# Performance work log

Hardware: AMD Instinct MI355X
Metric: run time of the kernel (lower is better)

The kernel has to match this reference:

```python
import jax, jax.numpy as jnp
import numpy as np

N, E, QL, HID = 1024, 8192, 8, 1024
NH, NKV, HD = 16, 8, 64          # heads, kv heads, head_dim; groups = NH // NKV = 2
INTER = 4096
THETA = 10000.0
EPS = 1e-6


def rmsnorm(x, w):
    v = x.astype(jnp.float32)
    v = v * jax.lax.rsqrt(jnp.mean(v * v, axis=-1, keepdims=True) + EPS)
    return w * v.astype(x.dtype)


def rotate_half(x):
    h = x.shape[-1] // 2
    return jnp.concatenate([-x[..., h:], x[..., :h]], axis=-1)


def rope_tables(seq_len):
    inv_freq = 1.0 / (THETA ** (jnp.arange(0, HD, 2, dtype=jnp.float32) / HD))
    freqs = jnp.arange(seq_len, dtype=jnp.float32)[:, None] * inv_freq[None, :]
    emb = jnp.concatenate([freqs, freqs], axis=-1)  # [seq_len, HD]
    return jnp.cos(emb), jnp.sin(emb)


def setup_inputs() -> dict:
    key = jax.random.key(0)
    ks = jax.random.split(key, 14)
    w = lambda k, sh: (jax.random.normal(k, sh, jnp.float32) * 0.02)
    return {
        "hidden_states": jax.random.normal(ks[0], (N, QL, HID), jnp.float32),
        "edge_index": jax.random.randint(ks[1], (2, E), 0, N, dtype=jnp.int32),
        "edge_hidden_states": jax.random.normal(ks[2], (E, QL, HID), jnp.float32),
        "Wq": w(ks[3], (NH * HD, HID)),
        "Wk": w(ks[4], (NKV * HD, HID)),
        "Wv": w(ks[5], (NKV * HD, HID)),
        "Wo": w(ks[6], (HID, HID)),
        "Wgate": w(ks[7], (INTER, HID)),
        "Wup": w(ks[8], (INTER, HID)),
        "Wdown": w(ks[9], (HID, INTER)),
        "ln1_w": jnp.ones((HID,), jnp.float32),
        "ln2_w": jnp.ones((HID,), jnp.float32),
    }


def gofa_layer(hidden_states, edge_index, edge_hidden_states, Wq, Wk, Wv, Wo,
               Wgate, Wup, Wdown, ln1_w, ln2_w):
    src, dst = edge_index[0], edge_index[1]  # message flows src -> dst
    residual = hidden_states
    x = rmsnorm(hidden_states, ln1_w)  # [N, QL, HID]

    q = x @ Wq.T                     # [N, QL, NH*HD]
    k = x @ Wk.T                     # [N, QL, NKV*HD]
    v = x @ Wv.T
    ek = edge_hidden_states @ Wk.T   # [E, QL, NKV*HD]
    ev = edge_hidden_states @ Wv.T

    # per-edge gather
    q_i = q[dst]                     # [E, QL, NH*HD]
    k_j, v_j = k[src], v[src]        # [E, QL, NKV*HD]

    # interleave node/edge tokens: [E, 2*QL, NKV*HD]
    keys = jnp.stack([k_j, ek], axis=2).reshape(E, 2 * QL, NKV * HD)
    vals = jnp.stack([v_j, ev], axis=2).reshape(E, 2 * QL, NKV * HD)

    qh = q_i.reshape(E, QL, NH, HD).transpose(0, 2, 1, 3)        # [E, NH, QL, HD]
    kh = keys.reshape(E, 2 * QL, NKV, HD).transpose(0, 2, 1, 3)  # [E, NKV, 2QL, HD]
    vh = vals.reshape(E, 2 * QL, NKV, HD).transpose(0, 2, 1, 3)

    cos_k, sin_k = rope_tables(2 * QL)
    cos_q, sin_q = cos_k[:QL], sin_k[:QL]
    qh = qh * cos_q[None, None] + rotate_half(qh) * sin_q[None, None]
    kh = kh * cos_k[None, None] + rotate_half(kh) * sin_k[None, None]

    groups = NH // NKV
    kh = jnp.repeat(kh, groups, axis=1)  # [E, NH, 2QL, HD]
    vh = jnp.repeat(vh, groups, axis=1)

    logits = jnp.einsum('ehqd,ehkd->ehqk', qh, kh) / np.sqrt(HD)  # [E, NH, QL, 2QL]

    # segment softmax over (edges into same dst node) x (2QL key positions)
    seg = jnp.repeat(dst, 2 * QL)                                  # [E*2QL]
    a = logits.transpose(0, 3, 1, 2).reshape(E * 2 * QL, NH, QL)   # [E*2QL, NH, QL]
    m = jax.ops.segment_max(a, seg, num_segments=N)                # [N, NH, QL]
    ex = jnp.exp(a - m[seg])
    s = jax.ops.segment_sum(ex, seg, num_segments=N)
    alpha = ex / (s[seg] + 1e-16)
    alpha = alpha.reshape(E, 2 * QL, NH, QL).transpose(0, 2, 3, 1)  # [E, NH, QL, 2QL]

    out_e = jnp.einsum('ehqk,ehkd->ehqd', alpha, vh)               # [E, NH, QL, HD]
    out_e = out_e.transpose(0, 2, 1, 3).reshape(E, QL, HID)

    agg = jax.ops.segment_sum(out_e, dst, num_segments=N)          # [N, QL, HID]
    attn_out = agg @ Wo.T

    h = residual + attn_out
    h2 = rmsnorm(h, ln2_w)
    mlp = (jax.nn.silu(h2 @ Wgate.T) * (h2 @ Wup.T)) @ Wdown.T
    return h + mlp


def reference(hidden_states, edge_index, edge_hidden_states, Wq, Wk, Wv, Wo,
              Wgate, Wup, Wdown, ln1_w, ln2_w):
    return gofa_layer(hidden_states, edge_index, edge_hidden_states, Wq, Wk, Wv,
                      Wo, Wgate, Wup, Wdown, ln1_w, ln2_w)
```

## Files before the change

kernel.cpp:

```cpp
#include <hip/hip_runtime.h>
#include <cstddef>
#include <cstdint>

constexpr int kN    = 1024;
constexpr int kE    = 8192;
constexpr int kQL   = 8;
constexpr int kHID  = 1024;

typedef __bf16 bf16x8 __attribute__((ext_vector_type(8)));
typedef float  f32x4  __attribute__((ext_vector_type(4)));
typedef unsigned short ushort8 __attribute__((ext_vector_type(8)));

__device__ __forceinline__ unsigned short f2bf(float f) {
  unsigned u = __float_as_uint(f);
  unsigned r = (u + 0x7FFFu + ((u >> 16) & 1u)) >> 16;
  return (unsigned short)r;
}
__device__ __forceinline__ float bf2f(unsigned short u) {
  return __uint_as_float((unsigned)u << 16);
}
__device__ __forceinline__ unsigned pkbf(float a, float b) {
  return (unsigned)f2bf(a) | ((unsigned)f2bf(b) << 16);
}
__device__ __forceinline__ void gload_lds16(const void* g, void* l) {
  __builtin_amdgcn_global_load_lds(
      (const __attribute__((address_space(1))) void*)g,
      (__attribute__((address_space(3))) void*)l, 16, 0, 0);
}

__global__ void rope_tables_kernel(float* __restrict__ ct, float* __restrict__ st) {
  int i = threadIdx.x;
  int p = i >> 5, j = i & 31;
  float inv = expf(-((float)(2 * j) / 64.0f) * logf(10000.0f));
  float ang = (float)p * inv;
  ct[i] = cosf(ang);
  st[i] = sinf(ang);
}

__global__ __launch_bounds__(256) void cvt_kernel(
    const float* __restrict__ in, unsigned short* __restrict__ out, int n8) {
  int i = blockIdx.x * 256 + threadIdx.x;
  if (i >= n8) return;
  const float4* p = (const float4*)(in + (size_t)i * 8);
  float4 a = p[0], b = p[1];
  uint4 o;
  o.x = f2bf(a.x) | ((unsigned)f2bf(a.y) << 16);
  o.y = f2bf(a.z) | ((unsigned)f2bf(a.w) << 16);
  o.z = f2bf(b.x) | ((unsigned)f2bf(b.y) << 16);
  o.w = f2bf(b.z) | ((unsigned)f2bf(b.w) << 16);
  *(uint4*)(out + (size_t)i * 8) = o;
}

__global__ __launch_bounds__(256) void cvt_gu_kernel(
    const float* __restrict__ Wg, const float* __restrict__ Wu,
    unsigned short* __restrict__ out) {
  int i = blockIdx.x * 256 + threadIdx.x;
  int n = i >> 7, ck = (i & 127) * 8;
  int isUp = (n >> 4) & 1;
  int srow = (n >> 6) * 32 + ((n >> 5) & 1) * 16 + (n & 15);
  const float* src = (isUp ? Wu : Wg) + (size_t)srow * 1024 + ck;
  const float4* p = (const float4*)src;
  float4 a = p[0], b = p[1];
  uint4 o;
  o.x = f2bf(a.x) | ((unsigned)f2bf(a.y) << 16);
  o.y = f2bf(a.z) | ((unsigned)f2bf(a.w) << 16);
  o.z = f2bf(b.x) | ((unsigned)f2bf(b.y) << 16);
  o.w = f2bf(b.z) | ((unsigned)f2bf(b.w) << 16);
  *(uint4*)(out + (size_t)n * 1024 + ck) = o;
}

__global__ __launch_bounds__(256) void rmsnorm_bf16_kernel(
    const float* __restrict__ in, const float* __restrict__ w,
    unsigned short* __restrict__ out) {
  __shared__ float red[4];
  int row = blockIdx.x, tid = threadIdx.x;
  const float* p = in + (size_t)row * kHID + tid * 4;
  float4 v = *(const float4*)p;
  float ss = v.x*v.x + v.y*v.y + v.z*v.z + v.w*v.w;
  #pragma unroll
  for (int off = 32; off > 0; off >>= 1) ss += __shfl_down(ss, off);
  int lane = tid & 63, wv = tid >> 6;
  if (lane == 0) red[wv] = ss;
  __syncthreads();
  float tot = red[0] + red[1] + red[2] + red[3];
  float rn = rsqrtf(tot * (1.0f / (float)kHID) + 1e-6f);
  float4 w4 = *(const float4*)(w + tid * 4);
  uint2 o;
  o.x = f2bf(v.x*rn*w4.x) | ((unsigned)f2bf(v.y*rn*w4.y) << 16);
  o.y = f2bf(v.z*rn*w4.z) | ((unsigned)f2bf(v.w*rn*w4.w) << 16);
  *(uint2*)(out + (size_t)row * kHID + tid * 4) = o;
}

template<int OUTMODE, int BN>
__global__ __launch_bounds__(512, 2) void gemm256(
    const unsigned short* __restrict__ A, const unsigned short* __restrict__ B,
    const float* __restrict__ resid, void* __restrict__ Cout,
    const float* __restrict__ ct, const float* __restrict__ st,
    int M, int N, int K) {
  constexpr int MI    = (BN == 256) ? 8 : 4;
  constexpr int SPANM = (BN == 256) ? 128 : 64;
  constexpr int ABUF  = 8192;
  constexpr int BBUF  = (BN == 256) ? 8192 : 4096;
  constexpr int LPS   = (BN == 256) ? 4 : 3;
  __shared__ unsigned short As[4 * ABUF];
  __shared__ unsigned short Bs[4 * BBUF];
  const int tid = threadIdx.x;
  const int lane = tid & 63, wid = tid >> 6;
  const int gx = gridDim.x;
  int id = blockIdx.y * gx + blockIdx.x;
  {
    const int nwg = gx * gridDim.y;
    const int cpx = nwg >> 3;
    id = (id & 7) * cpx + (id >> 3);
  }
  const int m0 = (id / gx) * 256, n0 = (id % gx) * BN;
  const int wr = (BN == 256) ? (wid >> 2) : (wid >> 1);
  const int wc = (BN == 256) ? (wid & 3)  : (wid & 1);
  const int l15 = lane & 15, lg = lane >> 4;
  const int NT = K >> 5;

  const int srow = tid >> 2;
  const int schunk = (tid & 3) ^ ((srow >> 1) & 3);
  const unsigned short* Agp = A + (size_t)(m0 + srow) * K + schunk * 8;
  const unsigned short* Bgp = B + (size_t)(n0 + srow) * K + schunk * 8;
  const size_t rowK128 = (size_t)128 * K;
  unsigned short* ldsA = As + wid * 512;
  unsigned short* ldsB = Bs + wid * 512;

#define STAGE(kt_, b_) {                                         \
    const int _k0 = (kt_) * 32;                                  \
    gload_lds16(Agp + _k0,           ldsA + (b_) * ABUF);        \
    gload_lds16(Agp + rowK128 + _k0, ldsA + (b_) * ABUF + 4096); \
    gload_lds16(Bgp + _k0,           ldsB + (b_) * BBUF);        \
    if (BN == 256)                                               \
      gload_lds16(Bgp + rowK128 + _k0, ldsB + (b_) * BBUF + 4096); \
  }

  f32x4 acc[MI][4] = {};
  STAGE(0, 0); STAGE(1, 1); STAGE(2, 2);

  const int rchunk8 = (lg ^ ((l15 >> 1) & 3)) * 8;
  int cur = 0;
  for (int kt = 0; kt < NT; ++kt) {
    if (kt < NT - 2)       asm volatile("s_waitcnt vmcnt(%0)" :: "i"(2 * LPS) : "memory");
    else if (kt == NT - 2) asm volatile("s_waitcnt vmcnt(%0)" :: "i"(LPS) : "memory");
    else                   asm volatile("s_waitcnt vmcnt(0)" ::: "memory");
    __builtin_amdgcn_sched_barrier(0);
    __builtin_amdgcn_s_barrier();
    __builtin_amdgcn_sched_barrier(0);
    if (kt + 3 < NT) STAGE(kt + 3, (kt + 3) & 3);

    const unsigned short* Ac = As + cur * ABUF + (wr * SPANM + l15) * 32 + rchunk8;
    const unsigned short* Bc = Bs + cur * BBUF + (wc * 64 + l15) * 32 + rchunk8;
    bf16x8 af[MI], bfr[4];
    #pragma unroll
    for (int mi = 0; mi < MI; ++mi) af[mi] = *(const bf16x8*)(Ac + mi * 512);
    #pragma unroll
    for (int nj = 0; nj < 4; ++nj) bfr[nj] = *(const bf16x8*)(Bc + nj * 512);
    __builtin_amdgcn_s_setprio(1);
    #pragma unroll
    for (int mi = 0; mi < MI; ++mi)
      #pragma unroll
      for (int nj = 0; nj < 4; ++nj)
        acc[mi][nj] = __builtin_amdgcn_mfma_f32_16x16x32_bf16(af[mi], bfr[nj], acc[mi][nj], 0, 0, 0);
    __builtin_amdgcn_s_setprio(0);
    cur = (cur + 1) & 3;
  }
#undef STAGE

  const int r0 = lg * 4;
  const int bc = n0 + wc * 64;
  #pragma unroll
  for (int mi = 0; mi < MI; ++mi) {
    #pragma unroll
    for (int r = 0; r < 4; ++r) {
      const size_t grow = (size_t)(m0 + wr * SPANM + mi * 16 + r0 + r);
      if (OUTMODE == 0) {
        #pragma unroll
        for (int nj = 0; nj < 4; ++nj) {
          const size_t gi = grow * N + (bc + nj * 16 + l15);
          float v = acc[mi][nj][r];
          if (resid) v += resid[gi];
          ((float*)Cout)[gi] = v;
        }
      } else if (OUTMODE == 2) {
        #pragma unroll
        for (int p = 0; p < 2; ++p) {
          float gv = acc[mi][2 * p][r], uv = acc[mi][2 * p + 1][r];
          float res = gv / (1.f + __expf(-gv)) * uv;
          ((unsigned short*)Cout)[grow * (size_t)(N >> 1) + (bc >> 1) + p * 16 + l15] = f2bf(res);
        }
      } else {
        bool doR = false; int pos = 0;
        if (OUTMODE == 3) { doR = bc < 512; pos = 2 * ((int)grow & 7) + 1; }
        if (OUTMODE == 4) {
          if (bc < 1024)      { doR = true; pos = (int)grow & 7; }
          else if (bc < 1536) { doR = true; pos = 2 * ((int)grow & 7); }
        }
        unsigned short* o16 = (unsigned short*)Cout;
        if (doR) {
          #pragma unroll
          for (int nj = 0; nj < 2; ++nj) {
            float a = acc[mi][nj][r], b = acc[mi][nj + 2][r];
            float c = ct[pos * 32 + nj * 16 + l15];
            float s = st[pos * 32 + nj * 16 + l15];
            o16[grow * N + bc + nj * 16 + l15]       = f2bf(a * c - b * s);
            o16[grow * N + bc + (nj + 2) * 16 + l15] = f2bf(b * c + a * s);
          }
        } else {
          #pragma unroll
          for (int nj = 0; nj < 4; ++nj)
            o16[grow * N + bc + nj * 16 + l15] = f2bf(acc[mi][nj][r]);
        }
      }
    }
  }
}

__global__ void csr_count_kernel(const int* __restrict__ dst, int* __restrict__ cnt) {
  int e = blockIdx.x * 256 + threadIdx.x;
  if (e < kE) atomicAdd(&cnt[dst[e]], 1);
}
__global__ __launch_bounds__(1024) void csr_scan_kernel(
    const int* __restrict__ cnt, int* __restrict__ start) {
  __shared__ int tmp[1024];
  int t = threadIdx.x;
  tmp[t] = cnt[t];
  __syncthreads();
  for (int off = 1; off < 1024; off <<= 1) {
    int add = (t >= off) ? tmp[t - off] : 0;
    __syncthreads();
    tmp[t] += add;
    __syncthreads();
  }
  start[t + 1] = tmp[t];
  if (t == 0) start[0] = 0;
}
__global__ void csr_scatter_kernel(const int* __restrict__ dst, const int* __restrict__ start,
                                   int* __restrict__ cursor, int* __restrict__ elist) {
  int e = blockIdx.x * 256 + threadIdx.x;
  if (e < kE) {
    int d = dst[e];
    int pos = atomicAdd(&cursor[d], 1);
    elist[start[d] + pos] = e;
  }
}

__global__ __launch_bounds__(256) void attn_mfma_kernel(
    const unsigned short* __restrict__ qkv,
    const unsigned short* __restrict__ ekv,
    const int* __restrict__ srcIdx, const int* __restrict__ elist,
    const int* __restrict__ start,
    unsigned short* __restrict__ aggb) {
  const int n = blockIdx.x >> 1;
  const int g = (blockIdx.x & 1) * 4 + (threadIdx.x >> 6);
  const int lane = threadIdx.x & 63;
  const int l15 = lane & 15, lg = lane >> 4;

  const int h = g * 2 + (l15 >> 3), q = l15 & 7;
  const unsigned short* qrow = qkv + ((size_t)n * 8 + q) * 2048 + h * 64 + lg * 8;
  const bf16x8 qf0 = *(const bf16x8*)qrow;
  const bf16x8 qf1 = *(const bf16x8*)(qrow + 32);

  float m = -3.4e38f, sh = 0.f;
  f32x4 oacc[4];
  #pragma unroll
  for (int t = 0; t < 4; ++t) oacc[t] = (f32x4){0.f, 0.f, 0.f, 0.f};

  const int kparity = l15 & 1;
  const int t_ = l15 >> 1;
  const int lgh = lg & 1;
  const int eS = lg >> 1;

  const int s0 = start[n], s1 = start[n + 1];
  for (int jj = s0; jj < s1; jj += 2) {
    const int e0 = elist[jj];
    const bool has1 = (jj + 1 < s1);
    const int e1 = has1 ? elist[jj + 1] : e0;
    const int sn0 = srcIdx[e0], sn1 = srcIdx[e1];

    const unsigned short* kr0 = kparity
        ? ekv + ((size_t)e0 * 8 + t_) * 1024 + g * 64 + lg * 8
        : qkv + ((size_t)sn0 * 8 + t_) * 2048 + 1024 + g * 64 + lg * 8;
    const unsigned short* kr1 = kparity
        ? ekv + ((size_t)e1 * 8 + t_) * 1024 + g * 64 + lg * 8
        : qkv + ((size_t)sn1 * 8 + t_) * 2048 + 1024 + g * 64 + lg * 8;
    bf16x8 ka0 = *(const bf16x8*)kr0, ka1 = *(const bf16x8*)(kr0 + 32);
    bf16x8 kc0 = *(const bf16x8*)kr1, kc1 = *(const bf16x8*)(kr1 + 32);

    const int evsel = eS ? e1 : e0;
    const int snsel = eS ? sn1 : sn0;
    const unsigned short* vn = qkv + ((size_t)snsel * 8 + lgh * 4) * 2048 + 1536 + g * 64;
    const unsigned short* ve = ekv + ((size_t)evsel * 8 + lgh * 4) * 1024 + 512 + g * 64;

    f32x4 z = (f32x4){0.f, 0.f, 0.f, 0.f};
    f32x4 sa = __builtin_amdgcn_mfma_f32_16x16x32_bf16(ka0, qf0, z, 0, 0, 0);
    sa       = __builtin_amdgcn_mfma_f32_16x16x32_bf16(ka1, qf1, sa, 0, 0, 0);
    f32x4 sb = __builtin_amdgcn_mfma_f32_16x16x32_bf16(kc0, qf0, z, 0, 0, 0);
    sb       = __builtin_amdgcn_mfma_f32_16x16x32_bf16(kc1, qf1, sb, 0, 0, 0);

    float l0[4], l1[4];
    float lmax = -3.4e38f;
    #pragma unroll
    for (int r = 0; r < 4; ++r) {
      l0[r] = sa[r] * 0.125f;
      l1[r] = has1 ? sb[r] * 0.125f : -3.4e38f;
      lmax = fmaxf(lmax, fmaxf(l0[r], l1[r]));
    }
    lmax = fmaxf(lmax, __shfl_xor(lmax, 16));
    lmax = fmaxf(lmax, __shfl_xor(lmax, 32));
    const float mnew = fmaxf(m, lmax);
    const float scale = __expf(m - mnew);
    float p0[4], p1[4], ps = 0.f;
    #pragma unroll
    for (int r = 0; r < 4; ++r) {
      p0[r] = __expf(l0[r] - mnew);
      p1[r] = __expf(l1[r] - mnew);
      ps += p0[r] + p1[r];
    }
    ps += __shfl_xor(ps, 16);
    ps += __shfl_xor(ps, 32);
    sh = sh * scale + ps;
    m = mnew;

    #pragma unroll
    for (int r = 0; r < 4; ++r) {
      float sr = __shfl(scale, lg * 4 + r);
      #pragma unroll
      for (int t = 0; t < 4; ++t) oacc[t][r] *= sr;
    }

    unsigned w00 = pkbf(p0[0], p0[1]), w01 = pkbf(p0[2], p0[3]);
    unsigned w10 = pkbf(p1[0], p1[1]), w11 = pkbf(p1[2], p1[3]);
    const int L1 = l15 + 32 * lgh, L2 = L1 + 16;
    unsigned a0 = __shfl(w00, L1), a1 = __shfl(w01, L1);
    unsigned a2 = __shfl(w00, L2), a3 = __shfl(w01, L2);
    unsigned b0 = __shfl(w10, L1), b1 = __shfl(w11, L1);
    unsigned b2 = __shfl(w10, L2), b3 = __shfl(w11, L2);
    uint4 wv;
    wv.x = eS ? b0 : a0; wv.y = eS ? b1 : a1;
    wv.z = eS ? b2 : a2; wv.w = eS ? b3 : a3;
    const bf16x8 pf = __builtin_bit_cast(bf16x8, wv);

    #pragma unroll
    for (int t = 0; t < 4; ++t) {
      const int col = t * 16 + l15;
      ushort8 vr;
      #pragma unroll
      for (int j = 0; j < 8; ++j)
        vr[j] = (j & 1) ? ve[(j >> 1) * 1024 + col] : vn[(j >> 1) * 2048 + col];
      const bf16x8 vf = __builtin_bit_cast(bf16x8, vr);
      oacc[t] = __builtin_amdgcn_mfma_f32_16x16x32_bf16(pf, vf, oacc[t], 0, 0, 0);
    }
  }

  #pragma unroll
  for (int r = 0; r < 4; ++r) {
    const float sr = __shfl(sh, lg * 4 + r);
    const float inv = 1.f / (sr + 1e-16f);
    const int hq = lg * 4 + r;
    const int hh = g * 2 + (hq >> 3), qq = hq & 7;
    unsigned short* op = aggb + ((size_t)n * 8 + qq) * 1024 + hh * 64 + l15;
    #pragma unroll
    for (int t = 0; t < 4; ++t) op[t * 16] = f2bf(oacc[t][r] * inv);
  }
}

extern "C" void kernel_launch(void* const* d_in, const int* in_sizes, int n_in,
                              void* d_out, int out_size, void* d_ws, size_t ws_size,
                              hipStream_t stream) {
  const float* hidden = (const float*)d_in[0];
  const int*   eidx   = (const int*)d_in[1];
  const float* ehid   = (const float*)d_in[2];
  const float* Wq     = (const float*)d_in[3];
  const float* Wk     = (const float*)d_in[4];
  const float* Wv     = (const float*)d_in[5];
  const float* Wo     = (const float*)d_in[6];
  const float* Wgate  = (const float*)d_in[7];
  const float* Wup    = (const float*)d_in[8];
  const float* Wdown  = (const float*)d_in[9];
  const float* ln1    = (const float*)d_in[10];
  const float* ln2    = (const float*)d_in[11];
  const int* srcIdx = eidx;
  const int* dstIdx = eidx + kE;

  char* wsb = (char*)d_ws;
  size_t off = 0;
  auto alloc = [&](size_t bytes) { char* p = wsb + off; off += (bytes + 255) & ~(size_t)255; return p; };
  unsigned short* eh16   = (unsigned short*)alloc(134217728);
  unsigned short* ekv16  = (unsigned short*)alloc(134217728);
  unsigned short* qkv16  = (unsigned short*)alloc(33554432);
  unsigned short* x16    = (unsigned short*)alloc(16777216);
  unsigned short* agg16  = (unsigned short*)alloc(16777216);
  float*          hbuf   = (float*)alloc(33554432);
  unsigned short* wqkv16 = (unsigned short*)alloc(4194304);
  unsigned short* wo16   = (unsigned short*)alloc(2097152);
  unsigned short* wgu16  = (unsigned short*)alloc(16777216);
  unsigned short* wd16   = (unsigned short*)alloc(8388608);
  int* cnt    = (int*)alloc(4096);
  int* cursor = (int*)alloc(4096);
  int* startb = (int*)alloc(4352);
  int* elist  = (int*)alloc(32768);
  float* ct   = (float*)alloc(2048);
  float* st   = (float*)alloc(2048);
  unsigned short* gm16 = ekv16;
  unsigned short* h216 = x16;
  float* outp = (float*)d_out;

  hipMemsetAsync(cnt, 0, 8192, stream);
  rope_tables_kernel<<<1, 512, 0, stream>>>(ct, st);

  cvt_kernel<<<32768, 256, 0, stream>>>(ehid,  eh16, 8388608);
  cvt_kernel<<<512,   256, 0, stream>>>(Wq,    wqkv16,                 131072);
  cvt_kernel<<<256,   256, 0, stream>>>(Wk,    wqkv16 + 1024 * 1024,   65536);
  cvt_kernel<<<256,   256, 0, stream>>>(Wv,    wqkv16 + 1536 * 1024,   65536);
  cvt_kernel<<<512,   256, 0, stream>>>(Wo,    wo16,                  131072);
  cvt_gu_kernel<<<4096, 256, 0, stream>>>(Wgate, Wup, wgu16);
  cvt_kernel<<<2048,  256, 0, stream>>>(Wdown, wd16,                  524288);

  csr_count_kernel<<<32, 256, 0, stream>>>(dstIdx, cnt);
  csr_scan_kernel<<<1, 1024, 0, stream>>>(cnt, startb);
  csr_scatter_kernel<<<32, 256, 0, stream>>>(dstIdx, startb, cursor, elist);

  rmsnorm_bf16_kernel<<<kN * kQL, 256, 0, stream>>>(hidden, ln1, x16);

  gemm256<4, 256><<<dim3(8, 32),  512, 0, stream>>>(x16,  wqkv16, nullptr, qkv16, ct, st, 8192, 2048, 1024);
  gemm256<3, 256><<<dim3(4, 256), 512, 0, stream>>>(eh16, wqkv16 + 1024 * 1024, nullptr, ekv16, ct, st, 65536, 1024, 1024);

  attn_mfma_kernel<<<2048, 256, 0, stream>>>(qkv16, ekv16, srcIdx, elist, startb, agg16);

  gemm256<0, 128><<<dim3(8, 32), 512, 0, stream>>>(agg16, wo16, hidden, hbuf, ct, st, 8192, 1024, 1024);

  rmsnorm_bf16_kernel<<<kN * kQL, 256, 0, stream>>>(hbuf, ln2, h216);
  gemm256<2, 256><<<dim3(32, 32), 512, 0, stream>>>(h216, wgu16, nullptr, gm16, ct, st, 8192, 8192, 1024);
  gemm256<0, 128><<<dim3(8, 32), 512, 0, stream>>>(gm16, wd16, hbuf, outp, ct, st, 8192, 1024, 4096);
}
```

Baseline: 796.9 us.

## Replace GEMM with 8-phase ping-pong pipeline using BK=64 and quadrant-split MFMA

Replaces the 4-stage BK=32 GEMM with a double-buffered BK=64 kernel. Each k-tile pair is split into eight phases that interleave LDS fragment loads, global-to-LDS staging of A/B halves, and quadrant MFMA blocks, with barriers around each phase. All GEMMs, including the Wo and down projections that previously used a 128-wide N tile, now use a 256x256 tile. That halves the grid for those two launches and raises per-block work. The goal is better overlap of memory and MFMA and fewer waits per k step, at the cost of more barriers and possibly lower occupancy or poorer load balance on the smaller GEMMs.

```diff
diff --git a/kernel.cpp b/kernel.cpp
--- a/kernel.cpp
+++ b/kernel.cpp
@@ -91,19 +91,14 @@
   *(uint2*)(out + (size_t)row * kHID + tid * 4) = o;
 }
 
-template<int OUTMODE, int BN>
-__global__ __launch_bounds__(512, 2) void gemm256(
+template<int OUTMODE>
+__global__ __launch_bounds__(512, 2) void gemm8p(
     const unsigned short* __restrict__ A, const unsigned short* __restrict__ B,
     const float* __restrict__ resid, void* __restrict__ Cout,
     const float* __restrict__ ct, const float* __restrict__ st,
     int M, int N, int K) {
-  constexpr int MI    = (BN == 256) ? 8 : 4;
-  constexpr int SPANM = (BN == 256) ? 128 : 64;
-  constexpr int ABUF  = 8192;
-  constexpr int BBUF  = (BN == 256) ? 8192 : 4096;
-  constexpr int LPS   = (BN == 256) ? 4 : 3;
-  __shared__ unsigned short As[4 * ABUF];
-  __shared__ unsigned short Bs[4 * BBUF];
+  __shared__ unsigned short As[2][2][128][64];
+  __shared__ unsigned short Bs[2][2][128][64];
   const int tid = threadIdx.x;
   const int lane = tid & 63, wid = tid >> 6;
   const int gx = gridDim.x;
@@ -113,68 +108,128 @@
     const int cpx = nwg >> 3;
     id = (id & 7) * cpx + (id >> 3);
   }
-  const int m0 = (id / gx) * 256, n0 = (id % gx) * BN;
-  const int wr = (BN == 256) ? (wid >> 2) : (wid >> 1);
-  const int wc = (BN == 256) ? (wid & 3)  : (wid & 1);
+  const int m0 = (id / gx) * 256, n0 = (id % gx) * 256;
+  const int wr = wid >> 2, wc = wid & 3;
   const int l15 = lane & 15, lg = lane >> 4;
-  const int NT = K >> 5;
-
-  const int srow = tid >> 2;
-  const int schunk = (tid & 3) ^ ((srow >> 1) & 3);
-  const unsigned short* Agp = A + (size_t)(m0 + srow) * K + schunk * 8;
-  const unsigned short* Bgp = B + (size_t)(n0 + srow) * K + schunk * 8;
-  const size_t rowK128 = (size_t)128 * K;
-  unsigned short* ldsA = As + wid * 512;
-  unsigned short* ldsB = Bs + wid * 512;
-
-#define STAGE(kt_, b_) {                                         \
-    const int _k0 = (kt_) * 32;                                  \
-    gload_lds16(Agp + _k0,           ldsA + (b_) * ABUF);        \
-    gload_lds16(Agp + rowK128 + _k0, ldsA + (b_) * ABUF + 4096); \
-    gload_lds16(Bgp + _k0,           ldsB + (b_) * BBUF);        \
-    if (BN == 256)                                               \
-      gload_lds16(Bgp + rowK128 + _k0, ldsB + (b_) * BBUF + 4096); \
-  }
-
-  f32x4 acc[MI][4] = {};
-  STAGE(0, 0); STAGE(1, 1); STAGE(2, 2);
-
-  const int rchunk8 = (lg ^ ((l15 >> 1) & 3)) * 8;
-  int cur = 0;
-  for (int kt = 0; kt < NT; ++kt) {
-    if (kt < NT - 2)       asm volatile("s_waitcnt vmcnt(%0)" :: "i"(2 * LPS) : "memory");
-    else if (kt == NT - 2) asm volatile("s_waitcnt vmcnt(%0)" :: "i"(LPS) : "memory");
-    else                   asm volatile("s_waitcnt vmcnt(0)" ::: "memory");
-    __builtin_amdgcn_sched_barrier(0);
-    __builtin_amdgcn_s_barrier();
-    __builtin_amdgcn_sched_barrier(0);
-    if (kt + 3 < NT) STAGE(kt + 3, (kt + 3) & 3);
-
-    const unsigned short* Ac = As + cur * ABUF + (wr * SPANM + l15) * 32 + rchunk8;
-    const unsigned short* Bc = Bs + cur * BBUF + (wc * 64 + l15) * 32 + rchunk8;
-    bf16x8 af[MI], bfr[4];
-    #pragma unroll
-    for (int mi = 0; mi < MI; ++mi) af[mi] = *(const bf16x8*)(Ac + mi * 512);
-    #pragma unroll
-    for (int nj = 0; nj < 4; ++nj) bfr[nj] = *(const bf16x8*)(Bc + nj * 512);
-    __builtin_amdgcn_s_setprio(1);
-    #pragma unroll
-    for (int mi = 0; mi < MI; ++mi)
-      #pragma unroll
-      for (int nj = 0; nj < 4; ++nj)
-        acc[mi][nj] = __builtin_amdgcn_mfma_f32_16x16x32_bf16(af[mi], bfr[nj], acc[mi][nj], 0, 0, 0);
-    __builtin_amdgcn_s_setprio(0);
-    cur = (cur + 1) & 3;
-  }
-#undef STAGE
+  const int swz = l15 & 7;
+  const int NT = K >> 6;
+
+  const int scol = ((lane & 7) ^ (lane >> 3)) * 8;
+  const unsigned short* Asrc = A + (size_t)(m0 + wid * 16 + (lane >> 3)) * K + scol;
+  const unsigned short* Bsrc = B + (size_t)(n0 + wid * 16 + (lane >> 3)) * K + scol;
+  const size_t rK8 = (size_t)8 * K, rK128 = (size_t)128 * K;
+  const int brow0 = (wc & 1) * 64;
+
+#define STAGEA(t_, h_, b_) do {                                              \
+    gload_lds16(Asrc + (size_t)(h_) * rK128 + (size_t)(t_) * 64,             \
+                (unsigned short*)&As[b_][h_][0][0] + (wid * 2 + 0) * 512);   \
+    gload_lds16(Asrc + (size_t)(h_) * rK128 + rK8 + (size_t)(t_) * 64,       \
+                (unsigned short*)&As[b_][h_][0][0] + (wid * 2 + 1) * 512);   \
+  } while (0)
+#define STAGEB(t_, h_, b_) do {                                              \
+    gload_lds16(Bsrc + (size_t)(h_) * rK128 + (size_t)(t_) * 64,             \
+                (unsigned short*)&Bs[b_][h_][0][0] + (wid * 2 + 0) * 512);   \
+    gload_lds16(Bsrc + (size_t)(h_) * rK128 + rK8 + (size_t)(t_) * 64,       \
+                (unsigned short*)&Bs[b_][h_][0][0] + (wid * 2 + 1) * 512);   \
+  } while (0)
+
+  bf16x8 afr[2][4], bfr[2][4];
+#define LOADA(b_, qm_) do {                                                  \
+    _Pragma("unroll") for (int kk = 0; kk < 2; ++kk)                         \
+    _Pragma("unroll") for (int mi = 0; mi < 4; ++mi)                         \
+      afr[kk][mi] = *(const bf16x8*)&As[b_][wr][((qm_) * 4 + mi) * 16 + l15] \
+                                       [((kk * 4 + lg) ^ swz) * 8];          \
+  } while (0)
+#define LOADB(b_, qn_) do {                                                  \
+    _Pragma("unroll") for (int kk = 0; kk < 2; ++kk)                         \
+    _Pragma("unroll") for (int nj = 0; nj < 2; ++nj)                         \
+      bfr[kk][(qn_) * 2 + nj] =                                              \
+        *(const bf16x8*)&Bs[b_][wc >> 1][brow0 + ((qn_) * 2 + nj) * 16 + l15]\
+                           [((kk * 4 + lg) ^ swz) * 8];                      \
+  } while (0)
+
+  f32x4 acc[8][4] = {};
+#define MFMAQ(qm_, qn_) do {                                                 \
+    __builtin_amdgcn_s_setprio(1);                                           \
+    _Pragma("unroll") for (int mi = 0; mi < 4; ++mi)                         \
+    _Pragma("unroll") for (int nj = 0; nj < 2; ++nj) {                       \
+      acc[(qm_) * 4 + mi][(qn_) * 2 + nj] =                                  \
+        __builtin_amdgcn_mfma_f32_16x16x32_bf16(afr[0][mi],                  \
+          bfr[0][(qn_) * 2 + nj], acc[(qm_) * 4 + mi][(qn_) * 2 + nj], 0,0,0);\
+      acc[(qm_) * 4 + mi][(qn_) * 2 + nj] =                                  \
+        __builtin_amdgcn_mfma_f32_16x16x32_bf16(afr[1][mi],                  \
+          bfr[1][(qn_) * 2 + nj], acc[(qm_) * 4 + mi][(qn_) * 2 + nj], 0,0,0);\
+    }                                                                        \
+    __builtin_amdgcn_s_setprio(0);                                           \
+  } while (0)
+
+#define BAR_PRE() do {                                                       \
+    __builtin_amdgcn_sched_barrier(0);                                       \
+    __builtin_amdgcn_s_barrier();                                            \
+    asm volatile("s_waitcnt lgkmcnt(0)" ::: "memory");                       \
+    __builtin_amdgcn_sched_barrier(0);                                       \
+  } while (0)
+#define BAR_POST() do {                                                      \
+    __builtin_amdgcn_sched_barrier(0);                                       \
+    __builtin_amdgcn_s_barrier();                                            \
+    __builtin_amdgcn_sched_barrier(0);                                       \
+  } while (0)
+
+  STAGEA(0, 0, 0); STAGEA(0, 1, 0); STAGEB(0, 0, 0); STAGEB(0, 1, 0);
+  STAGEB(1, 0, 1); STAGEB(1, 1, 1);
+  asm volatile("s_waitcnt vmcnt(4)" ::: "memory");
+  __builtin_amdgcn_sched_barrier(0);
+  __builtin_amdgcn_s_barrier();
+  __builtin_amdgcn_sched_barrier(0);
+
+  for (int t0 = 0; t0 < NT; t0 += 2) {
+    const bool more = (t0 + 2 < NT);
+    LOADA(0, 0); LOADB(0, 0);
+    STAGEA(t0 + 1, 0, 1);
+    BAR_PRE(); MFMAQ(0, 0); BAR_POST();
+    LOADB(0, 1);
+    STAGEA(t0 + 1, 1, 1);
+    BAR_PRE(); MFMAQ(0, 1); BAR_POST();
+    LOADA(0, 1);
+    if (more) STAGEB(t0 + 2, 0, 0);
+    BAR_PRE(); MFMAQ(1, 0); BAR_POST();
+    if (more) {
+      asm volatile("s_waitcnt vmcnt(2)" ::: "memory");
+      STAGEB(t0 + 2, 1, 0);
+    } else {
+      asm volatile("s_waitcnt vmcnt(0)" ::: "memory");
+    }
+    BAR_PRE(); MFMAQ(1, 1); BAR_POST();
+    LOADA(1, 0); LOADB(1, 0);
+    if (more) STAGEA(t0 + 2, 0, 0);
+    BAR_PRE(); MFMAQ(0, 0); BAR_POST();
+    LOADB(1, 1);
+    if (more) STAGEA(t0 + 2, 1, 0);
+    BAR_PRE(); MFMAQ(0, 1); BAR_POST();
+    LOADA(1, 1);
+    if (more) STAGEB(t0 + 3, 0, 1);
+    BAR_PRE(); MFMAQ(1, 0); BAR_POST();
+    if (more) {
+      asm volatile("s_waitcnt vmcnt(2)" ::: "memory");
+      STAGEB(t0 + 3, 1, 1);
+    }
+    BAR_PRE(); MFMAQ(1, 1); BAR_POST();
+  }
+#undef STAGEA
+#undef STAGEB
+#undef LOADA
+#undef LOADB
+#undef MFMAQ
+#undef BAR_PRE
+#undef BAR_POST
 
   const int r0 = lg * 4;
   const int bc = n0 + wc * 64;
   #pragma unroll
-  for (int mi = 0; mi < MI; ++mi) {
+  for (int mi = 0; mi < 8; ++mi) {
     #pragma unroll
     for (int r = 0; r < 4; ++r) {
-      const size_t grow = (size_t)(m0 + wr * SPANM + mi * 16 + r0 + r);
+      const size_t grow = (size_t)(m0 + wr * 128 + mi * 16 + r0 + r);
       if (OUTMODE == 0) {
         #pragma unroll
         for (int nj = 0; nj < 4; ++nj) {
@@ -424,14 +479,14 @@
 
   rmsnorm_bf16_kernel<<<kN * kQL, 256, 0, stream>>>(hidden, ln1, x16);
 
-  gemm256<4, 256><<<dim3(8, 32),  512, 0, stream>>>(x16,  wqkv16, nullptr, qkv16, ct, st, 8192, 2048, 1024);
-  gemm256<3, 256><<<dim3(4, 256), 512, 0, stream>>>(eh16, wqkv16 + 1024 * 1024, nullptr, ekv16, ct, st, 65536, 1024, 1024);
+  gemm8p<4><<<dim3(8, 32),  512, 0, stream>>>(x16,  wqkv16, nullptr, qkv16, ct, st, 8192, 2048, 1024);
+  gemm8p<3><<<dim3(4, 256), 512, 0, stream>>>(eh16, wqkv16 + 1024 * 1024, nullptr, ekv16, ct, st, 65536, 1024, 1024);
 
   attn_mfma_kernel<<<2048, 256, 0, stream>>>(qkv16, ekv16, srcIdx, elist, startb, agg16);
 
-  gemm256<0, 128><<<dim3(8, 32), 512, 0, stream>>>(agg16, wo16, hidden, hbuf, ct, st, 8192, 1024, 1024);
+  gemm8p<0><<<dim3(4, 32), 512, 0, stream>>>(agg16, wo16, hidden, hbuf, ct, st, 8192, 1024, 1024);
 
   rmsnorm_bf16_kernel<<<kN * kQL, 256, 0, stream>>>(hbuf, ln2, h216);
-  gemm256<2, 256><<<dim3(32, 32), 512, 0, stream>>>(h216, wgu16, nullptr, gm16, ct, st, 8192, 8192, 1024);
-  gemm256<0, 128><<<dim3(8, 32), 512, 0, stream>>>(gm16, wd16, hbuf, outp, ct, st, 8192, 1024, 4096);
-}
+  gemm8p<2><<<dim3(32, 32), 512, 0, stream>>>(h216, wgu16, nullptr, gm16, ct, st, 8192, 8192, 1024);
+  gemm8p<0><<<dim3(4, 32), 512, 0, stream>>>(gm16, wd16, hbuf, outp, ct, st, 8192, 1024, 4096);
+}
```

New measurement: 787.8 us. About the same (-1.1%).

## Shrink GEMM tiles to 128-wide N with triple buffering for higher occupancy

Applied to the files above, without the earlier changes.

Replaces the 256x256/256x128 GEMM kernel with a templated kernel that fixes the N tile at 128 and makes the M tile either 256 or 128. It uses three LDS buffers instead of four and raises launch bounds so four workgroups can share a CU. The grids are doubled to match the smaller tiles. The smaller shared memory and register footprint is meant to raise occupancy and spread work over more workgroups. In exchange, each workgroup reuses less data, issues more global loads per FLOP, and has a shallower prefetch pipeline.

```diff
diff --git a/kernel.cpp b/kernel.cpp
--- a/kernel.cpp
+++ b/kernel.cpp
@@ -91,19 +91,19 @@
   *(uint2*)(out + (size_t)row * kHID + tid * 4) = o;
 }
 
-template<int OUTMODE, int BN>
-__global__ __launch_bounds__(512, 2) void gemm256(
+template<int OUTMODE, int TM>
+__global__ __launch_bounds__(512, 4) void gemmk(
     const unsigned short* __restrict__ A, const unsigned short* __restrict__ B,
     const float* __restrict__ resid, void* __restrict__ Cout,
     const float* __restrict__ ct, const float* __restrict__ st,
     int M, int N, int K) {
-  constexpr int MI    = (BN == 256) ? 8 : 4;
-  constexpr int SPANM = (BN == 256) ? 128 : 64;
-  constexpr int ABUF  = 8192;
-  constexpr int BBUF  = (BN == 256) ? 8192 : 4096;
-  constexpr int LPS   = (BN == 256) ? 4 : 3;
-  __shared__ unsigned short As[4 * ABUF];
-  __shared__ unsigned short Bs[4 * BBUF];
+  constexpr int ABUFE = TM * 32;
+  constexpr int BBUFE = 128 * 32;
+  constexpr int WRS   = TM / 4;
+  constexpr int MI    = WRS / 16;
+  constexpr int LPS   = (TM == 256) ? 3 : 2;
+  __shared__ unsigned short As[3 * ABUFE];
+  __shared__ unsigned short Bs[3 * BBUFE];
   const int tid = threadIdx.x;
   const int lane = tid & 63, wid = tid >> 6;
   const int gx = gridDim.x;
@@ -113,58 +113,58 @@
     const int cpx = nwg >> 3;
     id = (id & 7) * cpx + (id >> 3);
   }
-  const int m0 = (id / gx) * 256, n0 = (id % gx) * BN;
-  const int wr = (BN == 256) ? (wid >> 2) : (wid >> 1);
-  const int wc = (BN == 256) ? (wid & 3)  : (wid & 1);
+  const int m0 = (id / gx) * TM, n0 = (id % gx) * 128;
+  const int wr = wid >> 1, wc = wid & 1;
   const int l15 = lane & 15, lg = lane >> 4;
   const int NT = K >> 5;
 
-  const int srow = tid >> 2;
-  const int schunk = (tid & 3) ^ ((srow >> 1) & 3);
-  const unsigned short* Agp = A + (size_t)(m0 + srow) * K + schunk * 8;
-  const unsigned short* Bgp = B + (size_t)(n0 + srow) * K + schunk * 8;
-  const size_t rowK128 = (size_t)128 * K;
-  unsigned short* ldsA = As + wid * 512;
-  unsigned short* ldsB = Bs + wid * 512;
-
-#define STAGE(kt_, b_) {                                         \
-    const int _k0 = (kt_) * 32;                                  \
-    gload_lds16(Agp + _k0,           ldsA + (b_) * ABUF);        \
-    gload_lds16(Agp + rowK128 + _k0, ldsA + (b_) * ABUF + 4096); \
-    gload_lds16(Bgp + _k0,           ldsB + (b_) * BBUF);        \
-    if (BN == 256)                                               \
-      gload_lds16(Bgp + rowK128 + _k0, ldsB + (b_) * BBUF + 4096); \
-  }
+  const int sr4 = lane >> 2, sc = lane & 3;
+  const int arow0 = (TM == 256) ? (wid * 32 + sr4) : (wid * 16 + sr4);
+  const int brow0 = wid * 16 + sr4;
+  const unsigned short* Asrc = A + (size_t)(m0 + arow0) * K + (sc ^ (arow0 & 3)) * 8;
+  const unsigned short* Bsrc = B + (size_t)(n0 + brow0) * K + (sc ^ (brow0 & 3)) * 8;
+  const size_t rK16 = (size_t)16 * K;
+
+#define STAGE(t_, b_) do {                                                   \
+    const size_t _k0 = (size_t)(t_) * 32;                                    \
+    if (TM == 256) {                                                         \
+      gload_lds16(Asrc + _k0,        As + (b_) * ABUFE + wid * 1024);        \
+      gload_lds16(Asrc + rK16 + _k0, As + (b_) * ABUFE + wid * 1024 + 512);  \
+    } else {                                                                 \
+      gload_lds16(Asrc + _k0,        As + (b_) * ABUFE + wid * 512);         \
+    }                                                                        \
+    gload_lds16(Bsrc + _k0,          Bs + (b_) * BBUFE + wid * 512);         \
+  } while (0)
 
   f32x4 acc[MI][4] = {};
-  STAGE(0, 0); STAGE(1, 1); STAGE(2, 2);
-
-  const int rchunk8 = (lg ^ ((l15 >> 1) & 3)) * 8;
-  int cur = 0;
-  for (int kt = 0; kt < NT; ++kt) {
-    if (kt < NT - 2)       asm volatile("s_waitcnt vmcnt(%0)" :: "i"(2 * LPS) : "memory");
-    else if (kt == NT - 2) asm volatile("s_waitcnt vmcnt(%0)" :: "i"(LPS) : "memory");
-    else                   asm volatile("s_waitcnt vmcnt(0)" ::: "memory");
+  STAGE(0, 0); STAGE(1, 1);
+
+  const int rck = (lg ^ (l15 & 3)) * 8;
+  int cur = 0, nx2 = 2;
+  for (int t = 0; t < NT; ++t) {
     __builtin_amdgcn_sched_barrier(0);
+    if (t + 1 < NT) asm volatile("s_waitcnt vmcnt(%0)" :: "i"(LPS) : "memory");
+    else            asm volatile("s_waitcnt vmcnt(0)" ::: "memory");
     __builtin_amdgcn_s_barrier();
     __builtin_amdgcn_sched_barrier(0);
-    if (kt + 3 < NT) STAGE(kt + 3, (kt + 3) & 3);
-
-    const unsigned short* Ac = As + cur * ABUF + (wr * SPANM + l15) * 32 + rchunk8;
-    const unsigned short* Bc = Bs + cur * BBUF + (wc * 64 + l15) * 32 + rchunk8;
-    bf16x8 af[MI], bfr[4];
-    #pragma unroll
-    for (int mi = 0; mi < MI; ++mi) af[mi] = *(const bf16x8*)(Ac + mi * 512);
-    #pragma unroll
-    for (int nj = 0; nj < 4; ++nj) bfr[nj] = *(const bf16x8*)(Bc + nj * 512);
+    if (t + 2 < NT) STAGE(t + 2, nx2);
+
+    const unsigned short* Ab = As + cur * ABUFE + (wr * WRS + l15) * 32 + rck;
+    const unsigned short* Bb = Bs + cur * BBUFE + (wc * 64 + l15) * 32 + rck;
+    bf16x8 af[MI], bf[4];
+    #pragma unroll
+    for (int mi = 0; mi < MI; ++mi) af[mi] = *(const bf16x8*)(Ab + mi * 512);
+    #pragma unroll
+    for (int nj = 0; nj < 4; ++nj) bf[nj] = *(const bf16x8*)(Bb + nj * 512);
     __builtin_amdgcn_s_setprio(1);
     #pragma unroll
     for (int mi = 0; mi < MI; ++mi)
       #pragma unroll
       for (int nj = 0; nj < 4; ++nj)
-        acc[mi][nj] = __builtin_amdgcn_mfma_f32_16x16x32_bf16(af[mi], bfr[nj], acc[mi][nj], 0, 0, 0);
+        acc[mi][nj] = __builtin_amdgcn_mfma_f32_16x16x32_bf16(af[mi], bf[nj], acc[mi][nj], 0, 0, 0);
     __builtin_amdgcn_s_setprio(0);
-    cur = (cur + 1) & 3;
+    cur = (cur == 2) ? 0 : cur + 1;
+    nx2 = (nx2 == 2) ? 0 : nx2 + 1;
   }
 #undef STAGE
 
@@ -174,7 +174,7 @@
   for (int mi = 0; mi < MI; ++mi) {
     #pragma unroll
     for (int r = 0; r < 4; ++r) {
-      const size_t grow = (size_t)(m0 + wr * SPANM + mi * 16 + r0 + r);
+      const size_t grow = (size_t)(m0 + wr * WRS + mi * 16 + r0 + r);
       if (OUTMODE == 0) {
         #pragma unroll
         for (int nj = 0; nj < 4; ++nj) {
@@ -424,14 +424,14 @@
 
   rmsnorm_bf16_kernel<<<kN * kQL, 256, 0, stream>>>(hidden, ln1, x16);
 
-  gemm256<4, 256><<<dim3(8, 32),  512, 0, stream>>>(x16,  wqkv16, nullptr, qkv16, ct, st, 8192, 2048, 1024);
-  gemm256<3, 256><<<dim3(4, 256), 512, 0, stream>>>(eh16, wqkv16 + 1024 * 1024, nullptr, ekv16, ct, st, 65536, 1024, 1024);
+  gemmk<4, 256><<<dim3(16, 32),  512, 0, stream>>>(x16,  wqkv16, nullptr, qkv16, ct, st, 8192, 2048, 1024);
+  gemmk<3, 256><<<dim3(8, 256), 512, 0, stream>>>(eh16, wqkv16 + 1024 * 1024, nullptr, ekv16, ct, st, 65536, 1024, 1024);
 
   attn_mfma_kernel<<<2048, 256, 0, stream>>>(qkv16, ekv16, srcIdx, elist, startb, agg16);
 
-  gemm256<0, 128><<<dim3(8, 32), 512, 0, stream>>>(agg16, wo16, hidden, hbuf, ct, st, 8192, 1024, 1024);
+  gemmk<0, 128><<<dim3(8, 64), 512, 0, stream>>>(agg16, wo16, hidden, hbuf, ct, st, 8192, 1024, 1024);
 
   rmsnorm_bf16_kernel<<<kN * kQL, 256, 0, stream>>>(hbuf, ln2, h216);
-  gemm256<2, 256><<<dim3(32, 32), 512, 0, stream>>>(h216, wgu16, nullptr, gm16, ct, st, 8192, 8192, 1024);
-  gemm256<0, 128><<<dim3(8, 32), 512, 0, stream>>>(gm16, wd16, hbuf, outp, ct, st, 8192, 1024, 4096);
-}
+  gemmk<2, 256><<<dim3(64, 32), 512, 0, stream>>>(h216, wgu16, nullptr, gm16, ct, st, 8192, 8192, 1024);
+  gemmk<0, 128><<<dim3(8, 64), 512, 0, stream>>>(gm16, wd16, hbuf, outp, ct, st, 8192, 1024, 4096);
+}
```

Result: faster. 720.0 us (-9.7%).
